# Kernel optimization log

Hardware: AMD Instinct MI355X
Metric: run time of the kernel (lower is better)

## Reference

```python
import jax, jax.numpy as jnp
import numpy as np

K = 10        # neighbors kept (after dropping self)
N_SEEDS = 20  # FPS seeds
H = 0.01      # repulsion bandwidth


def setup_inputs() -> dict:
    key = jax.random.key(0)
    pcs = jax.random.uniform(key, (16, 65536, 3), dtype=jnp.float32)
    return {"pcs": pcs}


def farthest_point_sample(xyz, npoint, key):
    """Iterative FPS. xyz: [B,N,C] -> centroids [B,npoint] (int)."""
    B, N, C = xyz.shape
    distance = jnp.full((B, N), 1e10, dtype=xyz.dtype)
    farthest = jax.random.randint(key, (B,), 0, N)
    bidx = jnp.arange(B)

    def step(carry, _):
        dist_min, far = carry
        centroid = xyz[bidx, far][:, None, :]              # [B,1,C]
        d = jnp.sum((xyz - centroid) ** 2, axis=-1)        # [B,N]
        dist_min = jnp.minimum(dist_min, d)
        return (dist_min, jnp.argmax(dist_min, axis=-1)), far

    _, cents = jax.lax.scan(step, (distance, farthest), None, length=npoint)
    return cents.T  # [B, npoint]


def reference(pcs):
    B, N, C = pcs.shape
    seeds = farthest_point_sample(pcs, N_SEEDS, jax.random.key(1))   # [B,S]
    seeds_value = jnp.take_along_axis(
        pcs, jnp.broadcast_to(seeds[:, :, None], (B, N_SEEDS, C)), axis=1
    )  # [B,S,3]
    diff = pcs[:, :, None, :] - seeds_value[:, None, :, :]           # [B,N,S,3]
    sq = jnp.sum(diff * diff, axis=-1)                               # [B,N,S]
    # safe L2 norm (exact zeros at seed-vs-itself)
    dist = jnp.where(sq == 0, 0.0, jnp.sqrt(jnp.where(sq == 0, 1.0, sq)))
    dist_sn = dist.transpose(0, 2, 1)                                # [B,S,N]
    # k+1 smallest distances per seed, ascending (torch.topk largest=False)
    neg_top, _ = jax.lax.top_k(-dist_sn, K + 1)                      # [B,S,K+1]
    top_dist_net = -neg_top[:, :, 1:]                                # drop self, [B,S,K]
    weights = jnp.exp(-(top_dist_net ** 2) / (H * H))
    repulsion = -top_dist_net * weights
    return repulsion.sum(axis=2).sum(axis=1).mean()
```

## Files before the change

### kernel.cpp

```cpp
#include <hip/hip_runtime.h>
#include <cstdint>
#include <cfloat>
#include <cmath>

#define NPTS 65536
#define NB 16
#define NS 20
#define KK 10
#define FPB 16
#define NSm1 (NS - 1)

struct InitIdx { int idx[NB]; };

static __device__ __forceinline__ unsigned long long
agent_ld(const unsigned long long* p) {
    return __hip_atomic_load(p, __ATOMIC_RELAXED, __HIP_MEMORY_SCOPE_AGENT);
}

#define INS11(L, SQ)                                                     \
    {                                                                    \
        _Pragma("unroll")                                                \
        for (int jj = 10; jj >= 1; --jj)                                 \
            L[jj] = __builtin_amdgcn_fmed3f(L[jj - 1], L[jj], (SQ));     \
        L[0] = fminf(L[0], (SQ));                                        \
    }

#define WAVEPOP11(L, DEST)                                               \
    for (int r = 0; r < 11; ++r) {                                       \
        float v = L[0];                                                  \
        _Pragma("unroll")                                                \
        for (int off = 32; off >= 1; off >>= 1)                          \
            v = fminf(v, __shfl_xor(v, off));                            \
        unsigned long long m = __ballot(L[0] == v);                      \
        if (lane == (int)__ffsll(m) - 1) {                               \
            _Pragma("unroll")                                            \
            for (int jj = 0; jj < 10; ++jj) L[jj] = L[jj + 1];           \
            L[10] = FLT_MAX;                                             \
        }                                                                \
        if (lane == 0) (DEST)[r] = v;                                    \
    }

__global__ __launch_bounds__(1024, 4) void fps_kernel(const float* __restrict__ pcs,
                                                      unsigned long long* __restrict__ fkey,
                                                      float* __restrict__ part,
                                                      InitIdx init) {
    const int u   = blockIdx.x;
    const int xcd = u & 7;
    const int k   = u >> 3;
    const int b   = 2 * xcd + (k >> 4);
    const int j   = k & 15;
    const int t   = threadIdx.x;
    const int lane = t & 63;
    const int w    = t >> 6;
    const float* __restrict__ base = pcs + (size_t)b * NPTS * 3;
    const int pbase = j * 4096 + t * 4;

    const float4* q4 = reinterpret_cast<const float4*>(base + (size_t)pbase * 3);
    float4 A = q4[0], Bv = q4[1], Cv = q4[2];
    float x[4] = { A.x, A.w, Bv.z, Cv.y };
    float y[4] = { A.y, Bv.x, Bv.w, Cv.z };
    float z[4] = { A.z, Bv.y, Cv.x, Cv.w };
    float dm[4] = { 1e10f, 1e10f, 1e10f, 1e10f };

    __shared__ float s_val[16];
    __shared__ int   s_idx[16];
    __shared__ int   s_far;
    __shared__ int   s_seeds[NS];

    int far = init.idx[b];

    for (int s = 0; s < NS; ++s) {
        if (t == 0) s_seeds[s] = far;
        if (s == NSm1) break;

        const float* c = base + (size_t)far * 3;
        const float cx = c[0], cy = c[1], cz = c[2];

        float bestv = -1.0f;
        int   besti = 0;
#pragma unroll
        for (int q = 0; q < 4; ++q) {
            float dx = __fsub_rn(x[q], cx);
            float dy = __fsub_rn(y[q], cy);
            float dz = __fsub_rn(z[q], cz);
            float d  = __fadd_rn(__fadd_rn(__fmul_rn(dx, dx), __fmul_rn(dy, dy)),
                                 __fmul_rn(dz, dz));
            dm[q] = fminf(dm[q], d);
            if (dm[q] > bestv) { bestv = dm[q]; besti = pbase + q; }
        }
#pragma unroll
        for (int off = 32; off >= 1; off >>= 1) {
            float ov = __shfl_down(bestv, off);
            int   oi = __shfl_down(besti, off);
            if (ov > bestv || (ov == bestv && oi < besti)) { bestv = ov; besti = oi; }
        }
        if (lane == 0) { s_val[w] = bestv; s_idx[w] = besti; }
        __syncthreads();

        if (w == 0) {
            unsigned long long kv = 0ULL;
            if (lane < 16) {
                kv = ((unsigned long long)__float_as_uint(s_val[lane]) << 32) |
                     (unsigned long long)(0xFFFFFFFFu - (unsigned int)s_idx[lane]);
            }
#pragma unroll
            for (int off = 8; off >= 1; off >>= 1) {
                unsigned int lo = (unsigned int)kv, hi = (unsigned int)(kv >> 32);
                unsigned int olo = (unsigned int)__shfl_xor((int)lo, off);
                unsigned int ohi = (unsigned int)__shfl_xor((int)hi, off);
                unsigned long long o = ((unsigned long long)ohi << 32) | olo;
                if (o > kv) kv = o;
            }
            unsigned long long* fp = fkey + (size_t)(b * NS + s) * FPB;
            if (lane == 0)
                __hip_atomic_store(&fp[j], kv, __ATOMIC_RELAXED,
                                   __HIP_MEMORY_SCOPE_AGENT);

            const unsigned long long* sl = fp + (lane & 15);
            unsigned long long p0 = agent_ld(sl);
            unsigned long long p1 = agent_ld(sl);
            unsigned long long p2 = agent_ld(sl);
            unsigned long long v;
            for (;;) {
                if (!__any(p0 == 0ULL)) { v = p0; break; }
                p0 = agent_ld(sl);
                if (!__any(p1 == 0ULL)) { v = p1; break; }
                p1 = agent_ld(sl);
                if (!__any(p2 == 0ULL)) { v = p2; break; }
                p2 = agent_ld(sl);
            }
#pragma unroll
            for (int off = 32; off >= 1; off >>= 1) {
                unsigned int lo = (unsigned int)v, hi = (unsigned int)(v >> 32);
                unsigned int olo = (unsigned int)__shfl_xor((int)lo, off);
                unsigned int ohi = (unsigned int)__shfl_xor((int)hi, off);
                unsigned long long o = ((unsigned long long)ohi << 32) | olo;
                if (o > v) v = o;
            }
            if (lane == 0)
                s_far = (int)(0xFFFFFFFFu - (unsigned int)(v & 0xFFFFFFFFull));
        }
        __syncthreads();
        far = s_far;
    }

    __syncthreads();
#pragma unroll
    for (int pass = 0; pass < 2; ++pass) {
        const int s2 = w + pass * 16;
        if (s2 >= NS) break;
        const int sidx = s_seeds[s2];
        const float ccx = base[(size_t)sidx * 3 + 0];
        const float ccy = base[(size_t)sidx * 3 + 1];
        const float ccz = base[(size_t)sidx * 3 + 2];

        float lst[11];
#pragma unroll
        for (int jj = 0; jj < 11; ++jj) lst[jj] = FLT_MAX;

        for (int i = 0; i < 16; ++i) {
            const int pt = j * 4096 + (i * 64 + lane) * 4;
            const float4* qq = reinterpret_cast<const float4*>(base + (size_t)pt * 3);
            float4 qa = qq[0], qb = qq[1], qc = qq[2];
            float px[4] = { qa.x, qa.w, qb.z, qc.y };
            float py[4] = { qa.y, qb.x, qb.w, qc.z };
            float pz[4] = { qa.z, qb.y, qc.x, qc.w };
#pragma unroll
            for (int q = 0; q < 4; ++q) {
                float dx = __fsub_rn(px[q], ccx);
                float dy = __fsub_rn(py[q], ccy);
                float dz = __fsub_rn(pz[q], ccz);
                float sq = __fadd_rn(__fadd_rn(__fmul_rn(dx, dx), __fmul_rn(dy, dy)),
                                     __fmul_rn(dz, dz));
                INS11(lst, sq);
            }
        }
        float* pr = part + ((size_t)(b * NS + s2) * FPB + j) * 11;
        WAVEPOP11(lst, pr);
    }
}

__global__ __launch_bounds__(64) void knn_merge(const float* __restrict__ part,
                                               float* __restrict__ out) {
    const int pair = blockIdx.x;
    const int lane = threadIdx.x;
    const float* flat = part + (size_t)pair * 176;
    float a0 = flat[lane];
    float a1 = flat[lane + 64];
    float a2 = (lane + 128 < 176) ? flat[lane + 128] : FLT_MAX;

    const float HH = (float)(0.01 * 0.01);
    float acc = 0.0f;
#pragma unroll
    for (int r = 0; r < 11; ++r) {
        float mymin = fminf(a0, fminf(a1, a2));
        float v = mymin;
#pragma unroll
        for (int off = 32; off >= 1; off >>= 1) v = fminf(v, __shfl_xor(v, off));
        unsigned long long m = __ballot(mymin == v);
        if (lane == (int)__ffsll(m) - 1) {
            if (a0 == v)      a0 = FLT_MAX;
            else if (a1 == v) a1 = FLT_MAX;
            else              a2 = FLT_MAX;
        }
        if (lane == 0 && r >= 1) {
            float sq = v;
            float d  = (sq == 0.0f) ? 0.0f : __fsqrt_rn(sq);
            float q2 = __fmul_rn(d, d);
            float wt = expf(__fdiv_rn(-q2, HH));
            acc = __fadd_rn(acc, -__fmul_rn(d, wt));
        }
    }
    if (lane == 0) atomicAdd(out, acc * 0.0625f);
}

static inline uint32_t rotl32(uint32_t x, uint32_t d) { return (x << d) | (x >> (32 - d)); }

static void tf2x32(uint32_t k0, uint32_t k1, uint32_t x0, uint32_t x1,
                   uint32_t& y0, uint32_t& y1) {
    const uint32_t ks[3] = { k0, k1, k0 ^ k1 ^ 0x1BD11BDAu };
    const uint32_t rotA[4] = { 13, 15, 26, 6 };
    const uint32_t rotB[4] = { 17, 29, 16, 24 };
    uint32_t v0 = x0 + ks[0], v1 = x1 + ks[1];
    for (int i = 0; i < 5; ++i) {
        const uint32_t* rot = (i % 2 == 0) ? rotA : rotB;
        for (int j = 0; j < 4; ++j) {
            v0 += v1;
            v1 = rotl32(v1, rot[j]);
            v1 ^= v0;
        }
        v0 += ks[(i + 1) % 3];
        v1 += ks[(i + 2) % 3] + (uint32_t)(i + 1);
    }
    y0 = v0; y1 = v1;
}

extern "C" void kernel_launch(void* const* d_in, const int* in_sizes, int n_in,
                              void* d_out, int out_size, void* d_ws, size_t ws_size,
                              hipStream_t stream) {
    const float* pcs = (const float*)d_in[0];
    float* out = (float*)d_out;

    unsigned long long* fkey = (unsigned long long*)((char*)d_ws + 2048);
    float* part              = (float*)((char*)d_ws + 49152);

    uint32_t k2_0, k2_1;
    tf2x32(0u, 1u, 0u, 1u, k2_0, k2_1);
    InitIdx init;
    for (int i = 0; i < NB; ++i) {
        uint32_t y0, y1;
        tf2x32(k2_0, k2_1, 0u, (uint32_t)i, y0, y1);
        init.idx[i] = (int)((y0 ^ y1) & 0xFFFFu);
    }

    hipMemsetAsync((char*)d_ws + 2048, 0, 40960, stream);
    hipMemsetAsync(d_out, 0, sizeof(float), stream);

    hipLaunchKernelGGL(fps_kernel, dim3(NB * FPB), dim3(1024), 0, stream,
                       pcs, fkey, part, init);
    hipLaunchKernelGGL(knn_merge, dim3(320), dim3(64), 0, stream,
                       part, out);
}
```

Measured before the change: 77.11 us.

## Fuse kNN merge into FPS kernel and stage block points in LDS

```diff
diff --git a/kernel.cpp b/kernel.cpp
--- a/kernel.cpp
+++ b/kernel.cpp
@@ -16,6 +16,10 @@
 agent_ld(const unsigned long long* p) {
     return __hip_atomic_load(p, __ATOMIC_RELAXED, __HIP_MEMORY_SCOPE_AGENT);
 }
+static __device__ __forceinline__ unsigned int
+agent_ld32(const unsigned int* p) {
+    return __hip_atomic_load(p, __ATOMIC_RELAXED, __HIP_MEMORY_SCOPE_AGENT);
+}
 
 #define INS11(L, SQ)                                                     \
     {                                                                    \
@@ -25,24 +29,10 @@
         L[0] = fminf(L[0], (SQ));                                        \
     }
 
-#define WAVEPOP11(L, DEST)                                               \
-    for (int r = 0; r < 11; ++r) {                                       \
-        float v = L[0];                                                  \
-        _Pragma("unroll")                                                \
-        for (int off = 32; off >= 1; off >>= 1)                          \
-            v = fminf(v, __shfl_xor(v, off));                            \
-        unsigned long long m = __ballot(L[0] == v);                      \
-        if (lane == (int)__ffsll(m) - 1) {                               \
-            _Pragma("unroll")                                            \
-            for (int jj = 0; jj < 10; ++jj) L[jj] = L[jj + 1];           \
-            L[10] = FLT_MAX;                                             \
-        }                                                                \
-        if (lane == 0) (DEST)[r] = v;                                    \
-    }
-
 __global__ __launch_bounds__(1024, 4) void fps_kernel(const float* __restrict__ pcs,
                                                       unsigned long long* __restrict__ fkey,
-                                                      float* __restrict__ part,
+                                                      unsigned int* __restrict__ part,
+                                                      float* __restrict__ out,
                                                       InitIdx init) {
     const int u   = blockIdx.x;
     const int xcd = u & 7;
@@ -66,6 +56,9 @@
     __shared__ int   s_idx[16];
     __shared__ int   s_far;
     __shared__ int   s_seeds[NS];
+    __shared__ float xs[4096];
+    __shared__ float ys[4096];
+    __shared__ float zs[4096];
 
     int far = init.idx[b];
 
@@ -144,7 +137,16 @@
         far = s_far;
     }
 
+    {
+        float4* xv = reinterpret_cast<float4*>(xs);
+        float4* yv = reinterpret_cast<float4*>(ys);
+        float4* zv = reinterpret_cast<float4*>(zs);
+        xv[t] = make_float4(x[0], x[1], x[2], x[3]);
+        yv[t] = make_float4(y[0], y[1], y[2], y[3]);
+        zv[t] = make_float4(z[0], z[1], z[2], z[3]);
+    }
     __syncthreads();
+
 #pragma unroll
     for (int pass = 0; pass < 2; ++pass) {
         const int s2 = w + pass * 16;
@@ -158,13 +160,15 @@
 #pragma unroll
         for (int jj = 0; jj < 11; ++jj) lst[jj] = FLT_MAX;
 
+        const float4* xv = reinterpret_cast<const float4*>(xs);
+        const float4* yv = reinterpret_cast<const float4*>(ys);
+        const float4* zv = reinterpret_cast<const float4*>(zs);
         for (int i = 0; i < 16; ++i) {
-            const int pt = j * 4096 + (i * 64 + lane) * 4;
-            const float4* qq = reinterpret_cast<const float4*>(base + (size_t)pt * 3);
-            float4 qa = qq[0], qb = qq[1], qc = qq[2];
-            float px[4] = { qa.x, qa.w, qb.z, qc.y };
-            float py[4] = { qa.y, qb.x, qb.w, qc.z };
-            float pz[4] = { qa.z, qb.y, qc.x, qc.w };
+            const int p4 = i * 64 + lane;
+            float4 qx = xv[p4], qy = yv[p4], qz = zv[p4];
+            float px[4] = { qx.x, qx.y, qx.z, qx.w };
+            float py[4] = { qy.x, qy.y, qy.z, qy.w };
+            float pz[4] = { qz.x, qz.y, qz.z, qz.w };
 #pragma unroll
             for (int q = 0; q < 4; ++q) {
                 float dx = __fsub_rn(px[q], ccx);
@@ -175,43 +179,61 @@
                 INS11(lst, sq);
             }
         }
-        float* pr = part + ((size_t)(b * NS + s2) * FPB + j) * 11;
-        WAVEPOP11(lst, pr);
-    }
-}
-
-__global__ __launch_bounds__(64) void knn_merge(const float* __restrict__ part,
-                                               float* __restrict__ out) {
-    const int pair = blockIdx.x;
-    const int lane = threadIdx.x;
-    const float* flat = part + (size_t)pair * 176;
-    float a0 = flat[lane];
-    float a1 = flat[lane + 64];
-    float a2 = (lane + 128 < 176) ? flat[lane + 128] : FLT_MAX;
-
-    const float HH = (float)(0.01 * 0.01);
-    float acc = 0.0f;
-#pragma unroll
-    for (int r = 0; r < 11; ++r) {
-        float mymin = fminf(a0, fminf(a1, a2));
-        float v = mymin;
-#pragma unroll
-        for (int off = 32; off >= 1; off >>= 1) v = fminf(v, __shfl_xor(v, off));
-        unsigned long long m = __ballot(mymin == v);
-        if (lane == (int)__ffsll(m) - 1) {
-            if (a0 == v)      a0 = FLT_MAX;
-            else if (a1 == v) a1 = FLT_MAX;
-            else              a2 = FLT_MAX;
-        }
-        if (lane == 0 && r >= 1) {
-            float sq = v;
-            float d  = (sq == 0.0f) ? 0.0f : __fsqrt_rn(sq);
-            float q2 = __fmul_rn(d, d);
-            float wt = expf(__fdiv_rn(-q2, HH));
-            acc = __fadd_rn(acc, -__fmul_rn(d, wt));
-        }
-    }
-    if (lane == 0) atomicAdd(out, acc * 0.0625f);
+        unsigned int* pr = part + ((size_t)(b * NS + s2) * FPB + j) * 11;
+        for (int r = 0; r < 11; ++r) {
+            float v = lst[0];
+#pragma unroll
+            for (int off = 32; off >= 1; off >>= 1) v = fminf(v, __shfl_xor(v, off));
+            unsigned long long m = __ballot(lst[0] == v);
+            if (lane == (int)__ffsll(m) - 1) {
+#pragma unroll
+                for (int jj = 0; jj < 10; ++jj) lst[jj] = lst[jj + 1];
+                lst[10] = FLT_MAX;
+            }
+            if (lane == 0)
+                __hip_atomic_store(&pr[r], __float_as_uint(v) + 1u,
+                                   __ATOMIC_RELAXED, __HIP_MEMORY_SCOPE_AGENT);
+        }
+    }
+
+    for (int s2 = j; s2 < NS; s2 += FPB) {
+        if (w == 0) {
+            const unsigned int* sl2 = part + (size_t)(b * NS + s2) * FPB * 11;
+            unsigned int k0 = 0, k1 = 0, k2 = (lane + 128 < 176) ? 0u : 1u;
+            do {
+                if (k0 == 0) k0 = agent_ld32(&sl2[lane]);
+                if (k1 == 0) k1 = agent_ld32(&sl2[lane + 64]);
+                if (k2 == 0) k2 = agent_ld32(&sl2[lane + 128]);
+            } while (__any(k0 == 0 || k1 == 0 || k2 == 0));
+            float a0 = __uint_as_float(k0 - 1u);
+            float a1 = __uint_as_float(k1 - 1u);
+            float a2 = (lane + 128 < 176) ? __uint_as_float(k2 - 1u) : FLT_MAX;
+
+            const float HH = (float)(0.01 * 0.01);
+            float acc = 0.0f;
+#pragma unroll
+            for (int r = 0; r < 11; ++r) {
+                float mymin = fminf(a0, fminf(a1, a2));
+                float v = mymin;
+#pragma unroll
+                for (int off = 32; off >= 1; off >>= 1) v = fminf(v, __shfl_xor(v, off));
+                unsigned long long m = __ballot(mymin == v);
+                if (lane == (int)__ffsll(m) - 1) {
+                    if (a0 == v)      a0 = FLT_MAX;
+                    else if (a1 == v) a1 = FLT_MAX;
+                    else              a2 = FLT_MAX;
+                }
+                if (lane == 0 && r >= 1) {
+                    float sq = v;
+                    float dd = (sq == 0.0f) ? 0.0f : __fsqrt_rn(sq);
+                    float q2 = __fmul_rn(dd, dd);
+                    float wt = expf(__fdiv_rn(-q2, HH));
+                    acc = __fadd_rn(acc, -__fmul_rn(dd, wt));
+                }
+            }
+            if (lane == 0) atomicAdd(out, acc * 0.0625f);
+        }
+    }
 }
 
 static inline uint32_t rotl32(uint32_t x, uint32_t d) { return (x << d) | (x >> (32 - d)); }
@@ -242,7 +264,7 @@
     float* out = (float*)d_out;
 
     unsigned long long* fkey = (unsigned long long*)((char*)d_ws + 2048);
-    float* part              = (float*)((char*)d_ws + 49152);
+    unsigned int* part       = (unsigned int*)((char*)d_ws + 49152);
 
     uint32_t k2_0, k2_1;
     tf2x32(0u, 1u, 0u, 1u, k2_0, k2_1);
@@ -253,11 +275,9 @@
         init.idx[i] = (int)((y0 ^ y1) & 0xFFFFu);
     }
 
-    hipMemsetAsync((char*)d_ws + 2048, 0, 40960, stream);
+    hipMemsetAsync((char*)d_ws + 2048, 0, 272384, stream);
     hipMemsetAsync(d_out, 0, sizeof(float), stream);
 
     hipLaunchKernelGGL(fps_kernel, dim3(NB * FPB), dim3(1024), 0, stream,
-                       pcs, fkey, part, init);
-    hipLaunchKernelGGL(knn_merge, dim3(320), dim3(64), 0, stream,
-                       part, out);
-}
+                       pcs, fkey, part, out, init);
+}
```

Result: faster. 73.00 us (median of 2 runs) (-5.3%).
